# Kernel tuning notes

Measured on AMD Instinct MI355X. Metric: run time of the kernel, lower is better.

The kernel has to match this reference:

```python
import jax, jax.numpy as jnp
import numpy as np

N, E, NG = 50000, 800000, 256          # nodes, edges, graphs
NODE, EDGE, HID, OUT = 64, 16, 64, 1   # feature dims
NUM_LAYERS = 3


def _lin(key, fan_in, fan_out):
    # torch Linear default init: U(-1/sqrt(fan_in), 1/sqrt(fan_in))
    kw, kb = jax.random.split(key)
    bound = 1.0 / np.sqrt(fan_in)
    W = jax.random.uniform(kw, (fan_in, fan_out), jnp.float32, -bound, bound)
    b = jax.random.uniform(kb, (fan_out,), jnp.float32, -bound, bound)
    return W, b


def setup_inputs() -> dict:
    key = jax.random.key(0)
    ks = jax.random.split(key, 8)
    x = jax.random.normal(ks[0], (N, NODE), jnp.float32)
    edge_attr = jax.random.normal(ks[1], (E, EDGE), jnp.float32)
    edge_index = jax.random.randint(ks[2], (2, E), 0, N, dtype=jnp.int32)
    batch = jnp.sort(jax.random.randint(ks[3], (N,), 0, NG, dtype=jnp.int32))
    W_nh, b_nh = _lin(ks[4], NODE, HID)                 # node_to_hidden
    W_mh, b_mh = _lin(ks[5], 2 * HID + EDGE, HID)       # message_to_hidden
    W_om, b_om = _lin(ks[6], 2 * HID + NODE, HID)       # outMsgLin
    W_out, b_out = _lin(ks[7], HID, OUT)                # outLin
    return {"x": x, "edge_attr": edge_attr,
            "W_nh": W_nh, "b_nh": b_nh, "W_mh": W_mh, "b_mh": b_mh,
            "W_om": W_om, "b_om": b_om, "W_out": W_out, "b_out": b_out,
            "edge_index": edge_index, "batch": batch}


def reference(x, edge_attr, W_nh, b_nh, W_mh, b_mh, W_om, b_om, W_out, b_out,
              edge_index, batch):
    # h0 = relu(node_to_hidden(x))
    h0 = jax.nn.relu(x @ W_nh + b_nh)                      # [N, HID]

    # add_self_loops: append N self edges, self-loop edge_attr filled with 1.0
    self_idx = jnp.arange(N, dtype=edge_index.dtype)
    src = jnp.concatenate([edge_index[0], self_idx])       # x_j index (source)
    dst = jnp.concatenate([edge_index[1], self_idx])       # x_i index (target)
    ea = jnp.concatenate([edge_attr,
                          jnp.ones((N, EDGE), edge_attr.dtype)], axis=0)

    # MPN: num_layers of gather-concat -> scatter-add -> linear + h0 -> relu
    h = h0
    for _ in range(NUM_LAYERS):
        msg = jnp.concatenate([h[dst], h[src], ea], axis=1)        # [E+N, 2H+EDGE]
        agg = jax.ops.segment_sum(msg, dst, num_segments=N)        # [N, 2H+EDGE]
        h = jax.nn.relu(agg @ W_mh + b_mh + h0)                    # [N, HID]

    # outMsg: message = concat[h_i, h_j, x_j], aggr add, update identity
    out_msg = jnp.concatenate([h[dst], h[src], x[src]], axis=1)    # [E+N, 2H+NODE]
    agg2 = jax.ops.segment_sum(out_msg, dst, num_segments=N)       # [N, 2H+NODE]

    out = jax.nn.relu(agg2 @ W_om + b_om)                          # [N, HID]
    pooled = jax.ops.segment_sum(out, batch, num_segments=NG)      # [NG, HID]
    return pooled @ W_out + b_out                                  # [NG, OUT]
```

## Files before the change

kernel.cpp:

```cpp
#include <hip/hip_runtime.h>
#include <hip/hip_fp16.h>

#define N_NODES 50000
#define N_EDGES 800000
#define NGRAPH  256
#define FDIM    64
#define EDIM    16
#define NT      (N_NODES / 16)
#define SH      8
#define M8      (N_NODES * SH)
#define NB8     ((M8 + 255) / 256)
#define CH8     ((NB8 + 255) / 256)

#define GRPS       8
#define GRP_BLOCKS 256
#define GRID_CF    (GRPS * GRP_BLOCKS)
#define NPG        ((N_NODES + GRPS - 1) / GRPS)

#define SRC_SHARD(s) ((s) >> 13)

using half8  = __attribute__((ext_vector_type(8))) _Float16;
using float4v = __attribute__((ext_vector_type(4))) float;

__device__ __forceinline__ unsigned hmul2u(unsigned a, __half2 m) {
    __half2 r = __hmul2(__builtin_bit_cast(__half2, a), m);
    return __builtin_bit_cast(unsigned, r);
}
__device__ __forceinline__ unsigned packf2(float a, float b) {
    return __builtin_bit_cast(unsigned, __floats2half2_rn(a, b));
}


__global__ __launch_bounds__(256) void k_count(const int* __restrict__ src,
                                               const int* __restrict__ dst,
                                               int* __restrict__ cnt8) {
    int grp = blockIdx.x & (GRPS - 1);
    int bi  = blockIdx.x >> 3;
    int lo = grp * NPG;
    int hi = lo + NPG; if (hi > N_NODES) hi = N_NODES;
    for (int e = bi * 256 + threadIdx.x; e < N_EDGES; e += GRP_BLOCKS * 256) {
        int d = dst[e];
        if (d >= lo && d < hi) atomicAdd(&cnt8[d * SH + SRC_SHARD(src[e])], 1);
    }
}

__global__ void k_cvt(const float* __restrict__ x, __half* __restrict__ x16,
                      const float* __restrict__ edge_attr, __half* __restrict__ ea16) {
    int t = blockIdx.x * blockDim.x + threadIdx.x;
    int stride = gridDim.x * blockDim.x;
    const float4* x4 = (const float4*)x;
    uint4* xo = (uint4*)x16;
    for (int i = t; i < N_NODES * FDIM / 8; i += stride) {
        float4 a = x4[i * 2], b = x4[i * 2 + 1];
        uint4 o;
        o.x = packf2(a.x, a.y); o.y = packf2(a.z, a.w);
        o.z = packf2(b.x, b.y); o.w = packf2(b.z, b.w);
        xo[i] = o;
    }
    const float4* e4 = (const float4*)edge_attr;
    uint4* eo = (uint4*)ea16;
    for (int i = t; i < N_EDGES * EDIM / 8; i += stride) {
        float4 a = e4[i * 2], b = e4[i * 2 + 1];
        uint4 o;
        o.x = packf2(a.x, a.y); o.y = packf2(a.z, a.w);
        o.z = packf2(b.x, b.y); o.w = packf2(b.z, b.w);
        eo[i] = o;
    }
}

__global__ void k_blksum(const int* __restrict__ cnt8, int* __restrict__ blksum) {
    __shared__ int red[4];
    int b = blockIdx.x, t = threadIdx.x;
    int idx = b * 256 + t;
    int s = (idx < M8) ? cnt8[idx] : 0;
#pragma unroll
    for (int off = 32; off > 0; off >>= 1) s += __shfl_down(s, off, 64);
    int lane = t & 63, wid = t >> 6;
    if (lane == 0) red[wid] = s;
    __syncthreads();
    if (t == 0) blksum[b] = red[0] + red[1] + red[2] + red[3];
}

__global__ void k_scanblk(const int* __restrict__ blksum, int* __restrict__ boff,
                          int* __restrict__ rowp8) {
    __shared__ int sh[256];
    int t = threadIdx.x;
    int base = t * CH8;
    int v[CH8];
    int s = 0;
#pragma unroll
    for (int i = 0; i < CH8; i++) {
        int idx = base + i;
        v[i] = (idx < NB8) ? blksum[idx] : 0;
        s += v[i];
    }
    sh[t] = s;
    __syncthreads();
    for (int off = 1; off < 256; off <<= 1) {
        int u = (t >= off) ? sh[t - off] : 0;
        __syncthreads();
        sh[t] += u;
        __syncthreads();
    }
    int run = (t == 0) ? 0 : sh[t - 1];
#pragma unroll
    for (int i = 0; i < CH8; i++) {
        int idx = base + i;
        if (idx < NB8) boff[idx] = run;
        run += v[i];
    }
    if (t == 255) rowp8[M8] = sh[255];
}

__global__ void k_rowp(const int* __restrict__ cnt8, const int* __restrict__ boff,
                       int* __restrict__ rowp8, int* __restrict__ cur8,
                       float* __restrict__ degf) {
    __shared__ int sh[256];
    int b = blockIdx.x, t = threadIdx.x;
    int idx = b * 256 + t;
    int v = (idx < M8) ? cnt8[idx] : 0;
    sh[t] = v;
    __syncthreads();
    for (int off = 1; off < 256; off <<= 1) {
        int u = (t >= off) ? sh[t - off] : 0;
        __syncthreads();
        sh[t] += u;
        __syncthreads();
    }
    if (idx < M8) {
        int excl = sh[t] - v + boff[b];
        rowp8[idx] = excl;
        cur8[idx]  = excl;
        if ((t & 7) == 7) {
            int start = (t >= 8) ? sh[t - 8] : 0;
            degf[b * 32 + (t >> 3)] = (float)(sh[t] - start + 1);
        }
    }
}

__global__ __launch_bounds__(256) void k_fill(const int* __restrict__ src,
                                              const int* __restrict__ dst,
                                              int* __restrict__ cur8,
                                              int* __restrict__ colsrc,
                                              int* __restrict__ coledge) {
    int grp = blockIdx.x & (GRPS - 1);
    int bi  = blockIdx.x >> 3;
    int lo = grp * NPG;
    int hi = lo + NPG; if (hi > N_NODES) hi = N_NODES;
    for (int e = bi * 256 + threadIdx.x; e < N_EDGES; e += GRP_BLOCKS * 256) {
        int d = dst[e];
        if (d >= lo && d < hi) {
            int s = src[e];
            int pos = atomicAdd(&cur8[d * SH + SRC_SHARD(s)], 1);
            colsrc[pos]  = s;
            coledge[pos] = e;
        }
    }
}

#define SROW 136

__global__ __launch_bounds__(256, 4) void k_gmv(
    const __half* __restrict__ hin16,
    const int* __restrict__ rowp8, const int* __restrict__ colsrc,
    const __half* __restrict__ base16, const float* __restrict__ degf,
    const float* __restrict__ Wmh, __half* __restrict__ hout16) {
    __shared__ __align__(16) _Float16 S[2][16 * SROW];
    int lane = threadIdx.x & 63, wid = threadIdx.x >> 6;
    int tile = wid >> 1, h = wid & 1;
    int t = blockIdx.x * 2 + tile;
    int tb = t * 16;
    int g = lane >> 3;
    int c = lane & 7;
    const uint4* h8 = (const uint4*)hin16;

    if (t < NT) {
        int m = h * 8 + g;
        int node = tb + m;
        int beg = rowp8[node * SH], end = rowp8[(node + 1) * SH];
        float a0 = 0, a1 = 0, a2 = 0, a3 = 0, a4 = 0, a5 = 0, a6 = 0, a7 = 0;
        for (int p = beg; p < end; p += 8) {
            int cidx = p + c; if (cidx > end - 1) cidx = end - 1;
            int vj = colsrc[cidx];
#pragma unroll
            for (int k = 0; k < 8; k++) {
                int j = __shfl(vj, g * 8 + k, 64);
                if (p + k < end) {
                    uint4 v = h8[(size_t)j * 8 + c];
                    float2 f0 = __half22float2(__builtin_bit_cast(__half2, v.x));
                    float2 f1 = __half22float2(__builtin_bit_cast(__half2, v.y));
                    float2 f2 = __half22float2(__builtin_bit_cast(__half2, v.z));
                    float2 f3 = __half22float2(__builtin_bit_cast(__half2, v.w));
                    a0 += f0.x; a1 += f0.y; a2 += f1.x; a3 += f1.y;
                    a4 += f2.x; a5 += f2.y; a6 += f3.x; a7 += f3.y;
                }
            }
        }
        uint4 hv = h8[(size_t)node * 8 + c];
        float dg = degf[node];
        __half dh = __float2half(dg);
        __half2 dh2 = __halves2half2(dh, dh);
        float2 f0 = __half22float2(__builtin_bit_cast(__half2, hv.x));
        float2 f1 = __half22float2(__builtin_bit_cast(__half2, hv.y));
        float2 f2 = __half22float2(__builtin_bit_cast(__half2, hv.z));
        float2 f3 = __half22float2(__builtin_bit_cast(__half2, hv.w));
        uint4 s2, s1;
        s2.x = packf2(a0 + f0.x, a1 + f0.y);
        s2.y = packf2(a2 + f1.x, a3 + f1.y);
        s2.z = packf2(a4 + f2.x, a5 + f2.y);
        s2.w = packf2(a6 + f3.x, a7 + f3.y);
        s1.x = hmul2u(hv.x, dh2); s1.y = hmul2u(hv.y, dh2);
        s1.z = hmul2u(hv.z, dh2); s1.w = hmul2u(hv.w, dh2);
        uint4* Sw = (uint4*)(&S[tile][m * SROW]);
        Sw[c]     = s2;
        Sw[8 + c] = s1;
    }
    __syncthreads();
    if (t >= NT) return;

    int n = lane & 15, quad = lane >> 4;
    half8 bfr[4][2];
#pragma unroll
    for (int kk = 0; kk < 4; kk++)
#pragma unroll
        for (int i = 0; i < 2; i++) {
            int nn = h * 2 + i;
            half8 tmp;
#pragma unroll
            for (int j = 0; j < 8; j++) {
                int kp = kk * 32 + quad * 8 + j;
                int krow = (kp < 64) ? (64 + kp) : (kp - 64);
                tmp[j] = (_Float16)Wmh[krow * FDIM + nn * 16 + n];
            }
            bfr[kk][i] = tmp;
        }
    float4v acc[2];
#pragma unroll
    for (int i = 0; i < 2; i++)
#pragma unroll
        for (int r = 0; r < 4; r++)
            acc[i][r] = __half2float(base16[(size_t)(tb + quad * 4 + r) * FDIM + (h * 2 + i) * 16 + n]);
    const _Float16* Sr = S[tile];
#pragma unroll
    for (int kk = 0; kk < 4; kk++) {
        half8 a = *(const half8*)(Sr + n * SROW + kk * 32 + quad * 8);
#pragma unroll
        for (int i = 0; i < 2; i++)
            acc[i] = __builtin_amdgcn_mfma_f32_16x16x32_f16(a, bfr[kk][i], acc[i], 0, 0, 0);
    }
#pragma unroll
    for (int i = 0; i < 2; i++)
#pragma unroll
        for (int r = 0; r < 4; r++)
            hout16[(size_t)(tb + quad * 4 + r) * FDIM + (h * 2 + i) * 16 + n] =
                __float2half(fmaxf(acc[i][r], 0.f));
}

__global__ __launch_bounds__(256, 4) void k_gout(
    const __half* __restrict__ hin16,
    const int* __restrict__ rowp8, const int* __restrict__ colsrc,
    const __half* __restrict__ obase16, const float* __restrict__ degf,
    const float* __restrict__ Wom, const float* __restrict__ Wout,
    float* __restrict__ sc) {
    __shared__ __align__(16) _Float16 S[2][16 * SROW];
    __shared__ float part[2][2][16];
    int lane = threadIdx.x & 63, wid = threadIdx.x >> 6;
    int tile = wid >> 1, h = wid & 1;
    int t = blockIdx.x * 2 + tile;
    int tb = t * 16;
    int g = lane >> 3;
    int c = lane & 7;
    const uint4* h8 = (const uint4*)hin16;

    if (t < NT) {
        int m = h * 8 + g;
        int node = tb + m;
        int beg = rowp8[node * SH], end = rowp8[(node + 1) * SH];
        float a0 = 0, a1 = 0, a2 = 0, a3 = 0, a4 = 0, a5 = 0, a6 = 0, a7 = 0;
        for (int p = beg; p < end; p += 8) {
            int cidx = p + c; if (cidx > end - 1) cidx = end - 1;
            int vj = colsrc[cidx];
#pragma unroll
            for (int k = 0; k < 8; k++) {
                int j = __shfl(vj, g * 8 + k, 64);
                if (p + k < end) {
                    uint4 v = h8[(size_t)j * 8 + c];
                    float2 f0 = __half22float2(__builtin_bit_cast(__half2, v.x));
                    float2 f1 = __half22float2(__builtin_bit_cast(__half2, v.y));
                    float2 f2 = __half22float2(__builtin_bit_cast(__half2, v.z));
                    float2 f3 = __half22float2(__builtin_bit_cast(__half2, v.w));
                    a0 += f0.x; a1 += f0.y; a2 += f1.x; a3 += f1.y;
                    a4 += f2.x; a5 += f2.y; a6 += f3.x; a7 += f3.y;
                }
            }
        }
        uint4 hv = h8[(size_t)node * 8 + c];
        float dg = degf[node];
        __half dh = __float2half(dg);
        __half2 dh2 = __halves2half2(dh, dh);
        float2 f0 = __half22float2(__builtin_bit_cast(__half2, hv.x));
        float2 f1 = __half22float2(__builtin_bit_cast(__half2, hv.y));
        float2 f2 = __half22float2(__builtin_bit_cast(__half2, hv.z));
        float2 f3 = __half22float2(__builtin_bit_cast(__half2, hv.w));
        uint4 s2, s1;
        s2.x = packf2(a0 + f0.x, a1 + f0.y);
        s2.y = packf2(a2 + f1.x, a3 + f1.y);
        s2.z = packf2(a4 + f2.x, a5 + f2.y);
        s2.w = packf2(a6 + f3.x, a7 + f3.y);
        s1.x = hmul2u(hv.x, dh2); s1.y = hmul2u(hv.y, dh2);
        s1.z = hmul2u(hv.z, dh2); s1.w = hmul2u(hv.w, dh2);
        uint4* Sw = (uint4*)(&S[tile][m * SROW]);
        Sw[c]     = s2;
        Sw[8 + c] = s1;
    }
    __syncthreads();

    int n = lane & 15, quad = lane >> 4;
    if (t < NT) {
        half8 bfr[4][2];
#pragma unroll
        for (int kk = 0; kk < 4; kk++)
#pragma unroll
            for (int i = 0; i < 2; i++) {
                int nn = h * 2 + i;
                half8 tmp;
#pragma unroll
                for (int j = 0; j < 8; j++) {
                    int kp = kk * 32 + quad * 8 + j;
                    int krow = (kp < 64) ? (64 + kp) : (kp - 64);
                    tmp[j] = (_Float16)Wom[krow * FDIM + nn * 16 + n];
                }
                bfr[kk][i] = tmp;
            }
        float wo0 = Wout[(h * 2 + 0) * 16 + n];
        float wo1 = Wout[(h * 2 + 1) * 16 + n];
        float4v acc[2];
#pragma unroll
        for (int i = 0; i < 2; i++)
#pragma unroll
            for (int r = 0; r < 4; r++)
                acc[i][r] = __half2float(obase16[(size_t)(tb + quad * 4 + r) * FDIM + (h * 2 + i) * 16 + n]);
        const _Float16* Sr = S[tile];
#pragma unroll
        for (int kk = 0; kk < 4; kk++) {
            half8 a = *(const half8*)(Sr + n * SROW + kk * 32 + quad * 8);
#pragma unroll
            for (int i = 0; i < 2; i++)
                acc[i] = __builtin_amdgcn_mfma_f32_16x16x32_f16(a, bfr[kk][i], acc[i], 0, 0, 0);
        }
#pragma unroll
        for (int r = 0; r < 4; r++) {
            float s = fmaxf(acc[0][r], 0.f) * wo0 + fmaxf(acc[1][r], 0.f) * wo1;
            s += __shfl_xor(s, 1, 64);
            s += __shfl_xor(s, 2, 64);
            s += __shfl_xor(s, 4, 64);
            s += __shfl_xor(s, 8, 64);
            if (n == 0) part[tile][h][quad * 4 + r] = s;
        }
    }
    __syncthreads();
    if (t < NT && h == 0 && lane < 16)
        sc[tb + lane] = part[tile][0][lane] + part[tile][1][lane];
}

#define SROW2 72
__global__ __launch_bounds__(256, 4) void k_gxob(
    const __half* __restrict__ x16, const __half* __restrict__ ea16,
    const int* __restrict__ rowp8, const int* __restrict__ colsrc,
    const int* __restrict__ coledge,
    const float* __restrict__ Wom, const float* __restrict__ bom,
    __half* __restrict__ obase16, float* __restrict__ ea) {
    __shared__ __align__(16) _Float16 S[2][16 * SROW2];
    int lane = threadIdx.x & 63, wid = threadIdx.x >> 6;
    int tile = wid >> 1, h = wid & 1;
    int t = blockIdx.x * 2 + tile;
    int tb = t * 16;
    int g = lane >> 3;
    int c = lane & 7;
    const uint4* h8 = (const uint4*)x16;
    const unsigned* eap = (const unsigned*)ea16;

    if (t < NT) {
        int m = h * 8 + g;
        int node = tb + m;
        int beg = rowp8[node * SH], end = rowp8[(node + 1) * SH];
        float a0 = 0, a1 = 0, a2 = 0, a3 = 0, a4 = 0, a5 = 0, a6 = 0, a7 = 0;
        float x0 = 0.f, x1 = 0.f;
        for (int p = beg; p < end; p += 8) {
            int cidx = p + c; if (cidx > end - 1) cidx = end - 1;
            int vs = colsrc[cidx];
            int ve = coledge[cidx];
#pragma unroll
            for (int k = 0; k < 8; k++) {
                int j = __shfl(vs, g * 8 + k, 64);
                int e = __shfl(ve, g * 8 + k, 64);
                if (p + k < end) {
                    uint4 v = h8[(size_t)j * 8 + c];
                    unsigned w = eap[(size_t)e * 8 + c];
                    float2 wf = __half22float2(__builtin_bit_cast(__half2, w));
                    float2 f0 = __half22float2(__builtin_bit_cast(__half2, v.x));
                    float2 f1 = __half22float2(__builtin_bit_cast(__half2, v.y));
                    float2 f2 = __half22float2(__builtin_bit_cast(__half2, v.z));
                    float2 f3 = __half22float2(__builtin_bit_cast(__half2, v.w));
                    a0 += f0.x; a1 += f0.y; a2 += f1.x; a3 += f1.y;
                    a4 += f2.x; a5 += f2.y; a6 += f3.x; a7 += f3.y;
                    x0 += wf.x; x1 += wf.y;
                }
            }
        }
        uint4 xv = h8[(size_t)node * 8 + c];
        float2 f0 = __half22float2(__builtin_bit_cast(__half2, xv.x));
        float2 f1 = __half22float2(__builtin_bit_cast(__half2, xv.y));
        float2 f2 = __half22float2(__builtin_bit_cast(__half2, xv.z));
        float2 f3 = __half22float2(__builtin_bit_cast(__half2, xv.w));
        uint4 sA;
        sA.x = packf2(a0 + f0.x, a1 + f0.y);
        sA.y = packf2(a2 + f1.x, a3 + f1.y);
        sA.z = packf2(a4 + f2.x, a5 + f2.y);
        sA.w = packf2(a6 + f3.x, a7 + f3.y);
        ((uint4*)(&S[tile][m * SROW2]))[c] = sA;
        ((float2*)ea)[(size_t)node * 8 + c] = make_float2(x0, x1);
    }
    __syncthreads();
    if (t >= NT) return;

    int n = lane & 15, quad = lane >> 4;
    half8 bfr[2][2];
#pragma unroll
    for (int kk = 0; kk < 2; kk++)
#pragma unroll
        for (int i = 0; i < 2; i++) {
            int nn = h * 2 + i;
            half8 tmp;
#pragma unroll
            for (int j = 0; j < 8; j++) {
                int kp = kk * 32 + quad * 8 + j;
                tmp[j] = (_Float16)Wom[(128 + kp) * FDIM + nn * 16 + n];
            }
            bfr[kk][i] = tmp;
        }
    float4v acc[2];
#pragma unroll
    for (int i = 0; i < 2; i++) {
        float b = bom[(h * 2 + i) * 16 + n];
#pragma unroll
        for (int r = 0; r < 4; r++) acc[i][r] = b;
    }
    const _Float16* Sr = S[tile];
#pragma unroll
    for (int kk = 0; kk < 2; kk++) {
        half8 a = *(const half8*)(Sr + n * SROW2 + kk * 32 + quad * 8);
#pragma unroll
        for (int i = 0; i < 2; i++)
            acc[i] = __builtin_amdgcn_mfma_f32_16x16x32_f16(a, bfr[kk][i], acc[i], 0, 0, 0);
    }
#pragma unroll
    for (int i = 0; i < 2; i++)
#pragma unroll
        for (int r = 0; r < 4; r++)
            obase16[(size_t)(tb + quad * 4 + r) * FDIM + (h * 2 + i) * 16 + n] =
                __float2half(acc[i][r]);
}

__global__ void k_h0base(const float* __restrict__ x, const float* __restrict__ ea,
                         const float* __restrict__ Wnh, const float* __restrict__ bnh,
                         const float* __restrict__ Wmh, const float* __restrict__ bmh,
                         __half* __restrict__ h0out16, __half* __restrict__ base16) {
    __shared__ __align__(16) float sx[4][FDIM];
    __shared__ __align__(16) float sea[4][EDIM];
    int lane = threadIdx.x & 63;
    int wid  = threadIdx.x >> 6;
    float wnh[FDIM], w3[EDIM];
#pragma unroll
    for (int m = 0; m < FDIM; m++) wnh[m] = Wnh[m * FDIM + lane];
    float csum = 0.f;
#pragma unroll
    for (int m = 0; m < EDIM; m++) {
        w3[m] = Wmh[(2 * FDIM + m) * FDIM + lane];
        csum += w3[m];
    }
    float bnhk = bnh[lane], bmhk = bmh[lane];
    int gw = blockIdx.x * 4 + wid;
    int nw = gridDim.x * 4;
    for (int i = gw; i < N_NODES; i += nw) {
        sx[wid][lane] = x[i * FDIM + lane];
        if (lane < EDIM) sea[wid][lane] = ea[i * EDIM + lane];
        float acc0 = bnhk, acc1 = 0.f, acc2 = 0.f, acc3 = 0.f;
        const float4* s4 = (const float4*)sx[wid];
#pragma unroll
        for (int m4 = 0; m4 < FDIM / 4; m4++) {
            float4 v = s4[m4];
            acc0 = fmaf(v.x, wnh[4 * m4 + 0], acc0);
            acc1 = fmaf(v.y, wnh[4 * m4 + 1], acc1);
            acc2 = fmaf(v.z, wnh[4 * m4 + 2], acc2);
            acc3 = fmaf(v.w, wnh[4 * m4 + 3], acc3);
        }
        float h0 = fmaxf((acc0 + acc2) + (acc1 + acc3), 0.f);
        float b0 = h0 + bmhk + csum, b1 = 0.f, b2 = 0.f, b3 = 0.f;
        const float4* e4 = (const float4*)sea[wid];
#pragma unroll
        for (int m4 = 0; m4 < EDIM / 4; m4++) {
            float4 v = e4[m4];
            b0 = fmaf(v.x, w3[4 * m4 + 0], b0);
            b1 = fmaf(v.y, w3[4 * m4 + 1], b1);
            b2 = fmaf(v.z, w3[4 * m4 + 2], b2);
            b3 = fmaf(v.w, w3[4 * m4 + 3], b3);
        }
        h0out16[i * FDIM + lane] = __float2half(h0);
        base16[i * FDIM + lane]  = __float2half((b0 + b2) + (b1 + b3));
    }
}

__global__ void k_pool(const float* __restrict__ sc, const int* __restrict__ batch,
                       const float* __restrict__ b_out, float* __restrict__ out) {
    __shared__ float red[4];
    int g = blockIdx.x, t = threadIdx.x;
    int lo = 0, hi = N_NODES;
    while (lo < hi) { int mid = (lo + hi) >> 1; if (batch[mid] < g) lo = mid + 1; else hi = mid; }
    int lo2 = lo, hi2 = N_NODES;
    while (lo2 < hi2) { int mid = (lo2 + hi2) >> 1; if (batch[mid] < g + 1) lo2 = mid + 1; else hi2 = mid; }
    float s = 0.f;
    for (int i = lo + t; i < lo2; i += 256) s += sc[i];
#pragma unroll
    for (int off = 32; off > 0; off >>= 1) s += __shfl_down(s, off, 64);
    int lane = t & 63, wid = t >> 6;
    if (lane == 0) red[wid] = s;
    __syncthreads();
    if (t == 0) out[g] = red[0] + red[1] + red[2] + red[3] + b_out[0];
}


extern "C" void kernel_launch(void* const* d_in, const int* in_sizes, int n_in,
                              void* d_out, int out_size, void* d_ws, size_t ws_size,
                              hipStream_t stream) {
    const float* x         = (const float*)d_in[0];
    const float* edge_attr = (const float*)d_in[1];
    const float* Wnh       = (const float*)d_in[2];
    const float* bnh       = (const float*)d_in[3];
    const float* Wmh       = (const float*)d_in[4];
    const float* bmh       = (const float*)d_in[5];
    const float* Wom       = (const float*)d_in[6];
    const float* bom       = (const float*)d_in[7];
    const float* Wout      = (const float*)d_in[8];
    const float* bout      = (const float*)d_in[9];
    const int*   eidx      = (const int*)d_in[10];
    const int*   batch     = (const int*)d_in[11];
    const int*   srcI = eidx;
    const int*   dstI = eidx + N_EDGES;
    float* out = (float*)d_out;
    (void)in_sizes; (void)n_in; (void)out_size;

    char* w = (char*)d_ws;
    size_t off = 0;
    auto take = [&](size_t b) -> void* {
        void* p = w + off;
        off = (off + b + 255) & ~(size_t)255;
        return p;
    };
    float*  ea     = (float*)take((size_t)N_NODES * EDIM * 4);
    int*    cnt8   = (int*)take((size_t)M8 * 4);
    int*    rowp8  = (int*)take((size_t)(M8 + 1) * 4);
    int*    cur8   = (int*)take((size_t)M8 * 4);
    float*  degf   = (float*)take((size_t)N_NODES * 4);
    int*    colsrc = (int*)take((size_t)N_EDGES * 4);
    int*    coledge= (int*)take((size_t)N_EDGES * 4);
    __half* ea16   = (__half*)take((size_t)N_EDGES * EDIM * 2);
    float*  sc     = (float*)take((size_t)N_NODES * 4);
    int*    blks   = (int*)take((size_t)NB8 * 4);
    int*    boff   = (int*)take((size_t)NB8 * 4);
    __half* x16    = (__half*)take((size_t)N_NODES * FDIM * 2);
    __half* hA16   = (__half*)take((size_t)N_NODES * FDIM * 2);
    __half* hB16   = (__half*)take((size_t)N_NODES * FDIM * 2);
    __half* base16 = (__half*)take((size_t)N_NODES * FDIM * 2);
    __half* obase16= (__half*)take((size_t)N_NODES * FDIM * 2);
    (void)ws_size;

    const int G2 = (NT + 1) / 2;

    hipMemsetAsync(cnt8, 0, (size_t)M8 * 4, stream);
    k_count<<<GRID_CF, 256, 0, stream>>>(srcI, dstI, cnt8);
    k_cvt<<<2048, 256, 0, stream>>>(x, x16, edge_attr, ea16);
    k_blksum<<<NB8, 256, 0, stream>>>(cnt8, blks);
    k_scanblk<<<1, 256, 0, stream>>>(blks, boff, rowp8);
    k_rowp<<<NB8, 256, 0, stream>>>(cnt8, boff, rowp8, cur8, degf);
    k_fill<<<GRID_CF, 256, 0, stream>>>(srcI, dstI, cur8, colsrc, coledge);

    k_gxob<<<G2, 256, 0, stream>>>(x16, ea16, rowp8, colsrc, coledge,
                                   Wom, bom, obase16, ea);
    k_h0base<<<2048, 256, 0, stream>>>(x, ea, Wnh, bnh, Wmh, bmh, hA16, base16);

    k_gmv<<<G2, 256, 0, stream>>>(hA16, rowp8, colsrc, base16, degf, Wmh, hB16);
    k_gmv<<<G2, 256, 0, stream>>>(hB16, rowp8, colsrc, base16, degf, Wmh, hA16);
    k_gmv<<<G2, 256, 0, stream>>>(hA16, rowp8, colsrc, base16, degf, Wmh, hB16);

    k_gout<<<G2, 256, 0, stream>>>(hB16, rowp8, colsrc, obase16, degf, Wom, Wout, sc);
    k_pool<<<NGRAPH, 256, 0, stream>>>(sc, batch, bout, out);
}
```

Baseline: 337.2 us.

## Fuse fp16 conversion and h0 computation into the CSR fill kernel

Merges the x/edge_attr fp16 conversion and the h0/base precompute into extra blocks of the fill kernel, so this independent work runs alongside the atomic-heavy CSR fill and two launches go away. The self-loop edge term of base is split out into a small follow-up kernel that reads base16 back and adds the edge-attr projection. In exchange, base makes an extra fp16 round trip, which adds rounding, and the fused kernel holds more registers, which may lower occupancy for the fill blocks.

```diff
diff --git a/kernel.cpp b/kernel.cpp
--- a/kernel.cpp
+++ b/kernel.cpp
@@ -16,6 +16,7 @@
 #define GRP_BLOCKS 256
 #define GRID_CF    (GRPS * GRP_BLOCKS)
 #define NPG        ((N_NODES + GRPS - 1) / GRPS)
+#define PREB       1024
 
 #define SRC_SHARD(s) ((s) >> 13)
 
@@ -44,30 +45,6 @@
     }
 }
 
-__global__ void k_cvt(const float* __restrict__ x, __half* __restrict__ x16,
-                      const float* __restrict__ edge_attr, __half* __restrict__ ea16) {
-    int t = blockIdx.x * blockDim.x + threadIdx.x;
-    int stride = gridDim.x * blockDim.x;
-    const float4* x4 = (const float4*)x;
-    uint4* xo = (uint4*)x16;
-    for (int i = t; i < N_NODES * FDIM / 8; i += stride) {
-        float4 a = x4[i * 2], b = x4[i * 2 + 1];
-        uint4 o;
-        o.x = packf2(a.x, a.y); o.y = packf2(a.z, a.w);
-        o.z = packf2(b.x, b.y); o.w = packf2(b.z, b.w);
-        xo[i] = o;
-    }
-    const float4* e4 = (const float4*)edge_attr;
-    uint4* eo = (uint4*)ea16;
-    for (int i = t; i < N_EDGES * EDIM / 8; i += stride) {
-        float4 a = e4[i * 2], b = e4[i * 2 + 1];
-        uint4 o;
-        o.x = packf2(a.x, a.y); o.y = packf2(a.z, a.w);
-        o.z = packf2(b.x, b.y); o.w = packf2(b.z, b.w);
-        eo[i] = o;
-    }
-}
-
 __global__ void k_blksum(const int* __restrict__ cnt8, int* __restrict__ blksum) {
     __shared__ int red[4];
     int b = blockIdx.x, t = threadIdx.x;
@@ -138,23 +115,96 @@
     }
 }
 
-__global__ __launch_bounds__(256) void k_fill(const int* __restrict__ src,
-                                              const int* __restrict__ dst,
-                                              int* __restrict__ cur8,
-                                              int* __restrict__ colsrc,
-                                              int* __restrict__ coledge) {
-    int grp = blockIdx.x & (GRPS - 1);
-    int bi  = blockIdx.x >> 3;
-    int lo = grp * NPG;
-    int hi = lo + NPG; if (hi > N_NODES) hi = N_NODES;
-    for (int e = bi * 256 + threadIdx.x; e < N_EDGES; e += GRP_BLOCKS * 256) {
-        int d = dst[e];
-        if (d >= lo && d < hi) {
-            int s = src[e];
-            int pos = atomicAdd(&cur8[d * SH + SRC_SHARD(s)], 1);
-            colsrc[pos]  = s;
-            coledge[pos] = e;
-        }
+__global__ __launch_bounds__(256) void k_fillpre(
+    const int* __restrict__ src, const int* __restrict__ dst,
+    int* __restrict__ cur8, int* __restrict__ colsrc, int* __restrict__ coledge,
+    const float* __restrict__ x, __half* __restrict__ x16,
+    const float* __restrict__ edge_attr, __half* __restrict__ ea16,
+    const float* __restrict__ Wnh, const float* __restrict__ bnh,
+    const float* __restrict__ Wmh, const float* __restrict__ bmh,
+    __half* __restrict__ hA16, __half* __restrict__ base16) {
+    if (blockIdx.x < GRID_CF) {
+        int grp = blockIdx.x & (GRPS - 1);
+        int bi  = blockIdx.x >> 3;
+        int lo = grp * NPG;
+        int hi = lo + NPG; if (hi > N_NODES) hi = N_NODES;
+        for (int e = bi * 256 + threadIdx.x; e < N_EDGES; e += GRP_BLOCKS * 256) {
+            int d = dst[e];
+            if (d >= lo && d < hi) {
+                int s = src[e];
+                int pos = atomicAdd(&cur8[d * SH + SRC_SHARD(s)], 1);
+                colsrc[pos]  = s;
+                coledge[pos] = e;
+            }
+        }
+        return;
+    }
+    int pb = blockIdx.x - GRID_CF;
+    int lane = threadIdx.x & 63;
+    int wid  = threadIdx.x >> 6;
+    __shared__ __align__(16) float sx[4][FDIM];
+    float wnh[FDIM];
+#pragma unroll
+    for (int m = 0; m < FDIM; m++) wnh[m] = Wnh[m * FDIM + lane];
+    float csum = 0.f;
+#pragma unroll
+    for (int m = 0; m < EDIM; m++) csum += Wmh[(2 * FDIM + m) * FDIM + lane];
+    float bnhk = bnh[lane];
+    float bpk  = bmh[lane] + csum;
+    for (int i = pb * 4 + wid; i < N_NODES; i += PREB * 4) {
+        float xv = x[i * FDIM + lane];
+        sx[wid][lane] = xv;
+        x16[i * FDIM + lane] = __float2half(xv);
+        float acc0 = bnhk, acc1 = 0.f, acc2 = 0.f, acc3 = 0.f;
+        const float4* s4 = (const float4*)sx[wid];
+#pragma unroll
+        for (int m4 = 0; m4 < FDIM / 4; m4++) {
+            float4 v = s4[m4];
+            acc0 = fmaf(v.x, wnh[4 * m4 + 0], acc0);
+            acc1 = fmaf(v.y, wnh[4 * m4 + 1], acc1);
+            acc2 = fmaf(v.z, wnh[4 * m4 + 2], acc2);
+            acc3 = fmaf(v.w, wnh[4 * m4 + 3], acc3);
+        }
+        float h0 = fmaxf((acc0 + acc2) + (acc1 + acc3), 0.f);
+        hA16[i * FDIM + lane]   = __float2half(h0);
+        base16[i * FDIM + lane] = __float2half(h0 + bpk);
+    }
+    const float4* e4 = (const float4*)edge_attr;
+    uint4* eo = (uint4*)ea16;
+    int t = pb * 256 + threadIdx.x;
+    for (int i = t; i < N_EDGES * EDIM / 8; i += PREB * 256) {
+        float4 a = e4[i * 2], b = e4[i * 2 + 1];
+        uint4 o;
+        o.x = packf2(a.x, a.y); o.y = packf2(a.z, a.w);
+        o.z = packf2(b.x, b.y); o.w = packf2(b.z, b.w);
+        eo[i] = o;
+    }
+}
+
+__global__ void k_baseadd(const float* __restrict__ ea, const float* __restrict__ Wmh,
+                          __half* __restrict__ base16) {
+    __shared__ __align__(16) float sea[4][EDIM];
+    int lane = threadIdx.x & 63;
+    int wid  = threadIdx.x >> 6;
+    float w3[EDIM];
+#pragma unroll
+    for (int m = 0; m < EDIM; m++) w3[m] = Wmh[(2 * FDIM + m) * FDIM + lane];
+    int gw = blockIdx.x * 4 + wid;
+    int nw = gridDim.x * 4;
+    for (int i = gw; i < N_NODES; i += nw) {
+        if (lane < EDIM) sea[wid][lane] = ea[i * EDIM + lane];
+        float b0 = __half2float(base16[(size_t)i * FDIM + lane]);
+        float b1 = 0.f, b2 = 0.f, b3 = 0.f;
+        const float4* e4 = (const float4*)sea[wid];
+#pragma unroll
+        for (int m4 = 0; m4 < EDIM / 4; m4++) {
+            float4 v = e4[m4];
+            b0 = fmaf(v.x, w3[4 * m4 + 0], b0);
+            b1 = fmaf(v.y, w3[4 * m4 + 1], b1);
+            b2 = fmaf(v.z, w3[4 * m4 + 2], b2);
+            b3 = fmaf(v.w, w3[4 * m4 + 3], b3);
+        }
+        base16[(size_t)i * FDIM + lane] = __float2half((b0 + b2) + (b1 + b3));
     }
 }
 
@@ -460,55 +510,6 @@
         for (int r = 0; r < 4; r++)
             obase16[(size_t)(tb + quad * 4 + r) * FDIM + (h * 2 + i) * 16 + n] =
                 __float2half(acc[i][r]);
-}
-
-__global__ void k_h0base(const float* __restrict__ x, const float* __restrict__ ea,
-                         const float* __restrict__ Wnh, const float* __restrict__ bnh,
-                         const float* __restrict__ Wmh, const float* __restrict__ bmh,
-                         __half* __restrict__ h0out16, __half* __restrict__ base16) {
-    __shared__ __align__(16) float sx[4][FDIM];
-    __shared__ __align__(16) float sea[4][EDIM];
-    int lane = threadIdx.x & 63;
-    int wid  = threadIdx.x >> 6;
-    float wnh[FDIM], w3[EDIM];
-#pragma unroll
-    for (int m = 0; m < FDIM; m++) wnh[m] = Wnh[m * FDIM + lane];
-    float csum = 0.f;
-#pragma unroll
-    for (int m = 0; m < EDIM; m++) {
-        w3[m] = Wmh[(2 * FDIM + m) * FDIM + lane];
-        csum += w3[m];
-    }
-    float bnhk = bnh[lane], bmhk = bmh[lane];
-    int gw = blockIdx.x * 4 + wid;
-    int nw = gridDim.x * 4;
-    for (int i = gw; i < N_NODES; i += nw) {
-        sx[wid][lane] = x[i * FDIM + lane];
-        if (lane < EDIM) sea[wid][lane] = ea[i * EDIM + lane];
-        float acc0 = bnhk, acc1 = 0.f, acc2 = 0.f, acc3 = 0.f;
-        const float4* s4 = (const float4*)sx[wid];
-#pragma unroll
-        for (int m4 = 0; m4 < FDIM / 4; m4++) {
-            float4 v = s4[m4];
-            acc0 = fmaf(v.x, wnh[4 * m4 + 0], acc0);
-            acc1 = fmaf(v.y, wnh[4 * m4 + 1], acc1);
-            acc2 = fmaf(v.z, wnh[4 * m4 + 2], acc2);
-            acc3 = fmaf(v.w, wnh[4 * m4 + 3], acc3);
-        }
-        float h0 = fmaxf((acc0 + acc2) + (acc1 + acc3), 0.f);
-        float b0 = h0 + bmhk + csum, b1 = 0.f, b2 = 0.f, b3 = 0.f;
-        const float4* e4 = (const float4*)sea[wid];
-#pragma unroll
-        for (int m4 = 0; m4 < EDIM / 4; m4++) {
-            float4 v = e4[m4];
-            b0 = fmaf(v.x, w3[4 * m4 + 0], b0);
-            b1 = fmaf(v.y, w3[4 * m4 + 1], b1);
-            b2 = fmaf(v.z, w3[4 * m4 + 2], b2);
-            b3 = fmaf(v.w, w3[4 * m4 + 3], b3);
-        }
-        h0out16[i * FDIM + lane] = __float2half(h0);
-        base16[i * FDIM + lane]  = __float2half((b0 + b2) + (b1 + b3));
-    }
 }
 
 __global__ void k_pool(const float* __restrict__ sc, const int* __restrict__ batch,
@@ -579,15 +580,16 @@
 
     hipMemsetAsync(cnt8, 0, (size_t)M8 * 4, stream);
     k_count<<<GRID_CF, 256, 0, stream>>>(srcI, dstI, cnt8);
-    k_cvt<<<2048, 256, 0, stream>>>(x, x16, edge_attr, ea16);
     k_blksum<<<NB8, 256, 0, stream>>>(cnt8, blks);
     k_scanblk<<<1, 256, 0, stream>>>(blks, boff, rowp8);
     k_rowp<<<NB8, 256, 0, stream>>>(cnt8, boff, rowp8, cur8, degf);
-    k_fill<<<GRID_CF, 256, 0, stream>>>(srcI, dstI, cur8, colsrc, coledge);
+    k_fillpre<<<GRID_CF + PREB, 256, 0, stream>>>(
+        srcI, dstI, cur8, colsrc, coledge,
+        x, x16, edge_attr, ea16, Wnh, bnh, Wmh, bmh, hA16, base16);
 
     k_gxob<<<G2, 256, 0, stream>>>(x16, ea16, rowp8, colsrc, coledge,
                                    Wom, bom, obase16, ea);
-    k_h0base<<<2048, 256, 0, stream>>>(x, ea, Wnh, bnh, Wmh, bmh, hA16, base16);
+    k_baseadd<<<1024, 256, 0, stream>>>(ea, Wmh, base16);
 
     k_gmv<<<G2, 256, 0, stream>>>(hA16, rowp8, colsrc, base16, degf, Wmh, hB16);
     k_gmv<<<G2, 256, 0, stream>>>(hB16, rowp8, colsrc, base16, degf, Wmh, hA16);
```

Measured after the change: 345.7 us. 1.03x slower.
